# Performance work log

Hardware: AMD Instinct MI355X
Metric: run time of the kernel (lower is better)

## Reference

```python
import jax, jax.numpy as jnp
import numpy as np

RU, RV = 6, 6
DU, DV = 2 * RU + 1, 2 * RV + 1  # 13, 13 displacement offsets
C = 32  # feat_channels (WipModule.c_feat)


def _conv(x, w, stride=1, pad=1):
    return jax.lax.conv_general_dilated(
        x, w, (stride, stride), [(pad, pad), (pad, pad)],
        dimension_numbers=('NCHW', 'OIHW', 'NCHW'))


def _deconv(x, w):
    # expressed as an lhs-dilated conv (kernel stored directly in OIHW conv layout).
    p = 4 - 1 - 1
    return jax.lax.conv_general_dilated(
        x, w, (1, 1), [(p, p), (p, p)], lhs_dilation=(2, 2),
        dimension_numbers=('NCHW', 'OIHW', 'NCHW'))


def _kaiming(key, shape):
    fan_in = shape[1] * shape[2] * shape[3]
    return jax.random.normal(key, shape, jnp.float32) * np.float32(np.sqrt(2.0 / fan_in))


def setup_inputs() -> dict:
    key = jax.random.key(0)
    ks = jax.random.split(key, 8)
    B, H, W = 1, 64, 128
    return {
        'fmap1': jax.random.normal(ks[0], (B, C, H, W), jnp.float32),
        'fmap2': jax.random.normal(ks[1], (B, C, H, W), jnp.float32),
        'w1': _kaiming(ks[2], (96, 2 * C, 3, 3)),
        'w2': _kaiming(ks[3], (128, 96, 3, 3)),
        'w3': _kaiming(ks[4], (128, 128, 3, 3)),
        'w4': _kaiming(ks[5], (64, 128, 3, 3)),
        'wd': _kaiming(ks[6], (32, 64, 4, 4)),
        'w5': _kaiming(ks[7], (1, 32, 3, 3)),
    }


def _build_mvol(fmap1, fmap2):
    # Vectorized form of the torch itertools.product loop: one padded gather
    # over all (du, dv) displacement windows instead of 169 slice-assignments.
    b, c, h, w = fmap1.shape
    padded = jnp.pad(fmap2, ((0, 0), (0, 0), (RV, RV), (RU, RU)))

    def window(i, j):
        # shifted(y, x) = fmap2[y + (j - RV), x + (i - RU)], zero outside bounds
        return jax.lax.dynamic_slice(padded, (0, 0, j, i), (b, c, h, w))

    shifted = jax.vmap(lambda i: jax.vmap(lambda j: window(i, j))(jnp.arange(DV)))(jnp.arange(DU))
    shifted = jnp.moveaxis(shifted, 2, 0)  # (b, du, dv, c, h, w)
    # valid mask: detached channel-sum of the warped fmap2 slice (matches torch)
    valid = (jax.lax.stop_gradient(shifted).sum(axis=3, keepdims=True) != 0)
    valid = valid.astype(fmap1.dtype)
    m1 = fmap1[:, None, None] * valid  # broadcast fmap1 over (du, dv)
    return jnp.concatenate([m1, shifted * valid], axis=3)  # (b, du, dv, 2c, h, w)


def reference(fmap1, fmap2, w1, w2, w3, w4, wd, w5):
    mvol = _build_mvol(fmap1, fmap2)
    b, du, dv, c2, h, w = mvol.shape
    # MatchingNet: fold (du, dv) into batch, conv stack down to 1 cost channel
    x = mvol.reshape(b * du * dv, c2, h, w)
    x = jax.nn.relu(_conv(x, w1))
    x = jax.nn.relu(_conv(x, w2, stride=2))  # (.., 128, h/2, w/2)
    x = jax.nn.relu(_conv(x, w3))
    x = jax.nn.relu(_conv(x, w4))
    x = jax.nn.relu(_deconv(x, wd))          # back to (h, w)
    x = _conv(x, w5)                          # cost, 1 channel
    return x.reshape(b, du, dv, h, w)
```

## Files before the change

### kernel.cpp

```cpp
#include <hip/hip_runtime.h>

#define NITEMS 169

typedef __attribute__((ext_vector_type(8))) __bf16 bf16x8;
typedef __attribute__((ext_vector_type(4))) float f32x4;
typedef __attribute__((ext_vector_type(8))) unsigned short u16x8;
typedef __attribute__((ext_vector_type(4))) unsigned short u16x4;

__device__ __forceinline__ unsigned short f2b(float x) {
  union { float f; unsigned u; } v; v.f = x;
  unsigned r = v.u + 0x7fffu + ((v.u >> 16) & 1u);
  return (unsigned short)(r >> 16);
}
__device__ __forceinline__ float b2f(unsigned short u) {
  union { unsigned u; float f; } v; v.u = ((unsigned)u) << 16;
  return v.f;
}

__global__ __launch_bounds__(256) void k_prepf(const float* __restrict__ f,
                                               unsigned short* __restrict__ fb) {
  const int pix = blockIdx.x * 256 + threadIdx.x;
  const int y = pix >> 7, x = pix & 127;
#pragma unroll
  for (int c = 0; c < 32; ++c)
    fb[(size_t)pix * 32 + c] = f2b(f[(c * 64 + y) * 128 + x]);
}

__global__ void k_prep3x3(const float* __restrict__ w, unsigned short* __restrict__ wp,
                          int Cout, int Cin) {
  int i = blockIdx.x * 256 + threadIdx.x;
  if (i >= Cout * Cin * 9) return;
  int kx = i % 3, t = i / 3;
  int ky = t % 3; t /= 3;
  int cin = t % Cin, cout = t / Cin;
  int tap = ky * 3 + kx;
  wp[(((cin >> 5) * 9 + tap) * Cout + cout) * 32 + (cin & 31)] = f2b(w[i]);
}

__global__ void k_prepwd(const float* __restrict__ w, unsigned short* __restrict__ wp) {
  int i = blockIdx.x * 256 + threadIdx.x;
  if (i >= 32 * 64 * 16) return;
  int kx = i & 3, ky = (i >> 2) & 3, ci = (i >> 4) & 63, cout = i >> 10;
  wp[(((((ci >> 5) * 4 + ky) * 4 + kx) * 32) + cout) * 32 + (ci & 31)] = f2b(w[i]);
}

__global__ __launch_bounds__(256) void k_z1(
    const unsigned short* __restrict__ f1b, const unsigned short* __restrict__ wp,
    float* __restrict__ z1) {
  const int oy0 = blockIdx.x * 2;
  constexpr int WI = 130;
  __shared__ __align__(16) unsigned short X[4][4][WI][8];
  const int wid = threadIdx.x >> 6, lane = threadIdx.x & 63;
  const int lm = lane & 15, lkg = lane >> 4, lk = lkg * 8;

  f32x4 acc[24];
#pragma unroll
  for (int t = 0; t < 24; ++t) acc[t] = f32x4{0.f, 0.f, 0.f, 0.f};

  for (int c = threadIdx.x; c < 4 * 4 * WI; c += 256) {
    const int cig = c & 3, t2 = c >> 2;
    const int col = t2 % WI, r = t2 / WI;
    const int iy = oy0 - 1 + r, ix = col - 1;
    u16x8 v = {0, 0, 0, 0, 0, 0, 0, 0};
    if ((unsigned)iy < 64u && (unsigned)ix < 128u)
      v = *(const u16x8*)&f1b[(size_t)(iy * 128 + ix) * 32 + cig * 8];
    *(u16x8*)&X[r][cig][col][0] = v;
  }
  __syncthreads();
#pragma unroll
  for (int tap = 0; tap < 9; ++tap) {
    const int ky = tap / 3, kx = tap % 3;
    bf16x8 bf[4];
#pragma unroll
    for (int j = 0; j < 4; ++j) {
      const int mt = wid * 4 + j, rw = mt >> 3, mtx = mt & 7;
      bf[j] = *(const bf16x8*)&X[rw + ky][lkg][mtx * 16 + lm + kx][0];
    }
#pragma unroll
    for (int i = 0; i < 6; ++i) {
      bf16x8 af = *(const bf16x8*)&wp[((0 * 9 + tap) * 96 + i * 16 + lm) * 32 + lk];
#pragma unroll
      for (int j = 0; j < 4; ++j)
        acc[i * 4 + j] =
            __builtin_amdgcn_mfma_f32_16x16x32_bf16(af, bf[j], acc[i * 4 + j], 0, 0, 0);
    }
  }
#pragma unroll
  for (int i = 0; i < 6; ++i)
#pragma unroll
    for (int j = 0; j < 4; ++j) {
      const int mt = wid * 4 + j, rw = mt >> 3, mtx = mt & 7;
      const int cout0 = i * 16 + lkg * 4;
      const int m = mtx * 16 + lm;
      *(f32x4*)&z1[(size_t)((oy0 + rw) * 128 + m) * 96 + cout0] = acc[i * 4 + j];
    }
}

__global__ __launch_bounds__(256) void k_z2e(
    const unsigned short* __restrict__ f2b_, const unsigned short* __restrict__ wp,
    float* __restrict__ z2e) {
  const int u = blockIdx.x;
  constexpr int WI = 194;
  __shared__ __align__(16) unsigned short X[3][4][WI][8];
  const int wid = threadIdx.x >> 6, lane = threadIdx.x & 63;
  const int lm = lane & 15, lkg = lane >> 4, lk = lkg * 8;

  f32x4 acc[18];
#pragma unroll
  for (int t = 0; t < 18; ++t) acc[t] = f32x4{0.f, 0.f, 0.f, 0.f};

  for (int c = threadIdx.x; c < 3 * 4 * WI; c += 256) {
    const int cig = c & 3, t2 = c >> 2;
    const int col = t2 % WI, r = t2 / WI;
    const int iy = u + r - 7, ix = col - 7;
    u16x8 v = {0, 0, 0, 0, 0, 0, 0, 0};
    if ((unsigned)iy < 64u && (unsigned)ix < 128u)
      v = *(const u16x8*)&f2b_[(size_t)(iy * 128 + ix) * 32 + cig * 8];
    *(u16x8*)&X[r][cig][col][0] = v;
  }
  __syncthreads();
#pragma unroll
  for (int tap = 0; tap < 9; ++tap) {
    const int ky = tap / 3, kx = tap % 3;
    bf16x8 bf[3];
#pragma unroll
    for (int j = 0; j < 3; ++j) {
      const int mt = wid * 3 + j;
      bf[j] = *(const bf16x8*)&X[ky][lkg][mt * 16 + lm + kx][0];
    }
#pragma unroll
    for (int i = 0; i < 6; ++i) {
      bf16x8 af = *(const bf16x8*)&wp[((1 * 9 + tap) * 96 + i * 16 + lm) * 32 + lk];
#pragma unroll
      for (int j = 0; j < 3; ++j)
        acc[i * 3 + j] =
            __builtin_amdgcn_mfma_f32_16x16x32_bf16(af, bf[j], acc[i * 3 + j], 0, 0, 0);
    }
  }
#pragma unroll
  for (int i = 0; i < 6; ++i)
#pragma unroll
    for (int j = 0; j < 3; ++j) {
      const int v = (wid * 3 + j) * 16 + lm;
      if (v < 140) {
        const int cout0 = i * 16 + lkg * 4;
        *(f32x4*)&z2e[(size_t)(u * 140 + v) * 96 + cout0] = acc[i * 3 + j];
      }
    }
}

__global__ __launch_bounds__(256) void k_crow(
    const unsigned short* __restrict__ f1b, const unsigned short* __restrict__ wp,
    float* __restrict__ crow) {
  const int dyi = blockIdx.x / 7, r = blockIdx.x % 7;
  const int dy = dyi - 6;
  const int ady = dy < 0 ? -dy : dy;
  if (dy == 0 || r >= ady + 1) return;
  const int rowlo = dy > 0 ? 63 - dy : 0;
  const int oy = rowlo + r;
  constexpr int WI = 130;
  __shared__ __align__(16) unsigned short X[3][4][WI][8];
  const int wid = threadIdx.x >> 6, lane = threadIdx.x & 63;
  const int lm = lane & 15, lkg = lane >> 4, lk = lkg * 8;

  f32x4 acc[12];
#pragma unroll
  for (int t = 0; t < 12; ++t) acc[t] = f32x4{0.f, 0.f, 0.f, 0.f};

  for (int c = threadIdx.x; c < 3 * 4 * WI; c += 256) {
    const int cig = c & 3, t2 = c >> 2;
    const int col = t2 % WI, rr = t2 / WI;
    const int iy = oy - 1 + rr, ix = col - 1;
    const bool band = dy > 0 ? (iy >= 64 - dy) : (iy < -dy);
    u16x8 v = {0, 0, 0, 0, 0, 0, 0, 0};
    if (band && (unsigned)iy < 64u && (unsigned)ix < 128u)
      v = *(const u16x8*)&f1b[(size_t)(iy * 128 + ix) * 32 + cig * 8];
    *(u16x8*)&X[rr][cig][col][0] = v;
  }
  __syncthreads();
#pragma unroll
  for (int tap = 0; tap < 9; ++tap) {
    const int ky = tap / 3, kx = tap % 3;
    bf16x8 bf[2];
#pragma unroll
    for (int j = 0; j < 2; ++j)
      bf[j] = *(const bf16x8*)&X[ky][lkg][(wid * 2 + j) * 16 + lm + kx][0];
#pragma unroll
    for (int i = 0; i < 6; ++i) {
      bf16x8 af = *(const bf16x8*)&wp[((0 * 9 + tap) * 96 + i * 16 + lm) * 32 + lk];
#pragma unroll
      for (int j = 0; j < 2; ++j)
        acc[i * 2 + j] =
            __builtin_amdgcn_mfma_f32_16x16x32_bf16(af, bf[j], acc[i * 2 + j], 0, 0, 0);
    }
  }
#pragma unroll
  for (int i = 0; i < 6; ++i)
#pragma unroll
    for (int j = 0; j < 2; ++j) {
      const int cout0 = i * 16 + lkg * 4;
      const int m = (wid * 2 + j) * 16 + lm;
      *(f32x4*)&crow[(size_t)((dyi * 8 + r) * 128 + m) * 96 + cout0] = acc[i * 2 + j];
    }
}

__global__ __launch_bounds__(256) void k_ccol(
    const unsigned short* __restrict__ f1b, const unsigned short* __restrict__ wp,
    float* __restrict__ ccol) {
  const int dxi = blockIdx.x;
  const int dx = dxi - 6;
  const int adx = dx < 0 ? -dx : dx;
  if (dx == 0) return;
  const int ccnt = adx + 1;
  const int collo = dx > 0 ? 127 - dx : 0;
  __shared__ __align__(16) unsigned short X2[9][66][32];
  const int wid = threadIdx.x >> 6, lane = threadIdx.x & 63;
  const int lm = lane & 15, lkg = lane >> 4, lk = lkg * 8;

  for (int t = threadIdx.x; t < 9 * 66 * 4; t += 256) {
    const int cig = t & 3, pos = t >> 2;
    const int rr = pos % 66, cc = pos / 66;
    const int iy = rr - 1, ix = collo - 1 + cc;
    const bool band = dx > 0 ? (ix >= 128 - dx) : (ix < -dx);
    u16x8 v = {0, 0, 0, 0, 0, 0, 0, 0};
    if (band && (unsigned)iy < 64u && (unsigned)ix < 128u)
      v = *(const u16x8*)&f1b[(size_t)(iy * 128 + ix) * 32 + cig * 8];
    *(u16x8*)&X2[cc][rr][cig * 8] = v;
  }
  __syncthreads();
  for (int c = 0; c < ccnt; ++c) {
    f32x4 acc[6];
#pragma unroll
    for (int i = 0; i < 6; ++i) acc[i] = f32x4{0.f, 0.f, 0.f, 0.f};
#pragma unroll
    for (int tap = 0; tap < 9; ++tap) {
      const int ky = tap / 3, kx = tap % 3;
      bf16x8 bf = *(const bf16x8*)&X2[c + kx][wid * 16 + lm + ky][lk];
#pragma unroll
      for (int i = 0; i < 6; ++i) {
        bf16x8 af = *(const bf16x8*)&wp[((0 * 9 + tap) * 96 + i * 16 + lm) * 32 + lk];
        acc[i] = __builtin_amdgcn_mfma_f32_16x16x32_bf16(af, bf, acc[i], 0, 0, 0);
      }
    }
    const int y = wid * 16 + lm;
#pragma unroll
    for (int i = 0; i < 6; ++i) {
      const int cout0 = i * 16 + lkg * 4;
      *(f32x4*)&ccol[(size_t)((dxi * 64 + y) * 8 + c) * 96 + cout0] = acc[i];
    }
  }
}

__device__ __forceinline__ float dot32(const unsigned short* __restrict__ xv,
                                       const unsigned short* __restrict__ wv) {
  float s = 0.f;
#pragma unroll
  for (int cg = 0; cg < 4; ++cg) {
    u16x8 a = *(const u16x8*)&xv[cg * 8];
    u16x8 b = *(const u16x8*)&wv[cg * 8];
#pragma unroll
    for (int e = 0; e < 8; ++e) s += b2f(a[e]) * b2f(b[e]);
  }
  return s;
}

__global__ __launch_bounds__(256) void k_ccorner(
    const unsigned short* __restrict__ f1b, const unsigned short* __restrict__ w1p,
    float* __restrict__ ccor) {
  const int idx = blockIdx.x * 256 + threadIdx.x;
  if (idx >= NITEMS * 64 * 96) return;
  const int co = idx % 96, t = idx / 96;
  const int c = t & 7, r = (t >> 3) & 7, item = t >> 6;
  const int dx = item / 13 - 6, dy = item % 13 - 6;
  if (dx == 0 || dy == 0) return;
  const int ady = dy < 0 ? -dy : dy, adx = dx < 0 ? -dx : dx;
  if (r >= ady + 1 || c >= adx + 1) return;
  const int rowlo = dy > 0 ? 63 - dy : 0;
  const int collo = dx > 0 ? 127 - dx : 0;
  const int oy = rowlo + r, ox = collo + c;
  float acc = 0.f;
#pragma unroll
  for (int ky = 0; ky < 3; ++ky)
#pragma unroll
    for (int kx = 0; kx < 3; ++kx) {
      const int iy = oy - 1 + ky, ix = ox - 1 + kx;
      const bool rb = dy > 0 ? (iy >= 64 - dy) : (iy < -dy);
      const bool cb = dx > 0 ? (ix >= 128 - dx) : (ix < -dx);
      if (rb && cb && (unsigned)iy < 64u && (unsigned)ix < 128u)
        acc += dot32(&f1b[(size_t)(iy * 128 + ix) * 32],
                     &w1p[((ky * 3 + kx) * 96 + co) * 32]);
    }
  ccor[(size_t)(((item * 8 + r) * 8 + c) * 96) + co] = acc;
}

__global__ __launch_bounds__(256) void k_bcorr_rows(
    const unsigned short* __restrict__ f2bp, const unsigned short* __restrict__ w1p,
    float* __restrict__ rtop, float* __restrict__ rbot) {
  const int idx = blockIdx.x * 256 + threadIdx.x;
  if (idx >= 13 * 140 * 96) return;
  const int co = idx % 96, t = idx / 96;
  const int v = t % 140, dyi = t / 140;
  const int dy = dyi - 6;
  const int rt = dy - 1, rb = 64 + dy;
  float at = 0.f, ab = 0.f;
#pragma unroll
  for (int kx = 0; kx < 3; ++kx) {
    const int x2 = v - 7 + kx;
    if ((unsigned)x2 >= 128u) continue;
    if ((unsigned)rt < 64u)
      at += dot32(&f2bp[(size_t)(rt * 128 + x2) * 32],
                  &w1p[((9 + 0 + kx) * 96 + co) * 32]);
    if ((unsigned)rb < 64u)
      ab += dot32(&f2bp[(size_t)(rb * 128 + x2) * 32],
                  &w1p[((9 + 6 + kx) * 96 + co) * 32]);
  }
  rtop[idx] = at;
  rbot[idx] = ab;
}

__global__ __launch_bounds__(256) void k_bcorr_cols(
    const unsigned short* __restrict__ f2bp, const unsigned short* __restrict__ w1p,
    float* __restrict__ clft, float* __restrict__ crgt) {
  const int idx = blockIdx.x * 256 + threadIdx.x;
  if (idx >= 13 * 76 * 96) return;
  const int co = idx % 96, t = idx / 96;
  const int u = t % 76, dxi = t / 76;
  const int dx = dxi - 6;
  const int cl = dx - 1, cr = 128 + dx;
  float al = 0.f, ar = 0.f;
#pragma unroll
  for (int ky = 0; ky < 3; ++ky) {
    const int y2 = u - 7 + ky;
    if ((unsigned)y2 >= 64u) continue;
    if ((unsigned)cl < 128u)
      al += dot32(&f2bp[(size_t)(y2 * 128 + cl) * 32],
                  &w1p[((9 + ky * 3 + 0) * 96 + co) * 32]);
    if ((unsigned)cr < 128u)
      ar += dot32(&f2bp[(size_t)(y2 * 128 + cr) * 32],
                  &w1p[((9 + ky * 3 + 2) * 96 + co) * 32]);
  }
  clft[idx] = al;
  crgt[idx] = ar;
}

__global__ __launch_bounds__(256) void k_bcorr_corn(
    const unsigned short* __restrict__ f2bp, const unsigned short* __restrict__ w1p,
    float* __restrict__ kcorn) {
  const int idx = blockIdx.x * 256 + threadIdx.x;
  if (idx >= NITEMS * 4 * 96) return;
  const int co = idx % 96, t = idx / 96;
  const int corner = t % 4, item = t / 4;
  const int dx = item / 13 - 6, dy = item % 13 - 6;
  const int row = (corner < 2) ? dy - 1 : 64 + dy;
  const int col = (corner & 1) ? 128 + dx : dx - 1;
  const int ky = (corner < 2) ? 0 : 2;
  const int kx = (corner & 1) ? 2 : 0;
  float acc = 0.f;
  if ((unsigned)row < 64u && (unsigned)col < 128u)
    acc = dot32(&f2bp[(size_t)(row * 128 + col) * 32],
                &w1p[((9 + ky * 3 + kx) * 96 + co) * 32]);
  kcorn[idx] = acc;
}

__global__ __launch_bounds__(256) void k_assemble(
    const float* __restrict__ z1, const float* __restrict__ z2e,
    const float* __restrict__ crow, const float* __restrict__ ccol,
    const float* __restrict__ ccor, const float* __restrict__ rtop,
    const float* __restrict__ rbot, const float* __restrict__ clft,
    const float* __restrict__ crgt, const float* __restrict__ kcorn,
    unsigned short* __restrict__ x1, int base) {
  const int y = blockIdx.x, g = blockIdx.y, item = base + g;
  const int dx = item / 13 - 6, dy = item % 13 - 6;
  const int dyi = dy + 6, dxi = dx + 6;
  const int ady = dy < 0 ? -dy : dy, adx = dx < 0 ? -dx : dx;
  const int rowlo = dy > 0 ? 63 - dy : 0;
  const int rowhi = rowlo + (dy ? ady + 1 : 0);
  const int collo = dx > 0 ? 127 - dx : 0;
  const int colhi = collo + (dx ? adx + 1 : 0);
  const bool inrow = (y >= rowlo) && (y < rowhi);
  const int vrow = y + dy + 6;
  unsigned short* op = x1 + (size_t)g * (8192 * 96);

  for (int t = threadIdx.x; t < 128 * 24; t += 256) {
    const int px = t / 24, c0 = (t % 24) * 4;
    const int v = px + dx + 6;
    f32x4 s = *(const f32x4*)&z1[(size_t)(y * 128 + px) * 96 + c0];
    s += *(const f32x4*)&z2e[(size_t)(vrow * 140 + v) * 96 + c0];
    if (inrow)
      s -= *(const f32x4*)&crow[(size_t)((dyi * 8 + y - rowlo) * 128 + px) * 96 + c0];
    if (px >= collo && px < colhi) {
      s -= *(const f32x4*)&ccol[(size_t)((dxi * 64 + y) * 8 + px - collo) * 96 + c0];
      if (inrow)
        s += *(const f32x4*)&ccor[(size_t)(((item * 8 + y - rowlo) * 8) + px - collo) * 96 + c0];
    }
    if (y == 0) s -= *(const f32x4*)&rtop[(size_t)(dyi * 140 + v) * 96 + c0];
    if (y == 63) s -= *(const f32x4*)&rbot[(size_t)(dyi * 140 + v) * 96 + c0];
    if (px == 0) s -= *(const f32x4*)&clft[(size_t)(dxi * 76 + vrow) * 96 + c0];
    if (px == 127) s -= *(const f32x4*)&crgt[(size_t)(dxi * 76 + vrow) * 96 + c0];
    if (y == 0 && px == 0) s += *(const f32x4*)&kcorn[(size_t)item * 384 + 0 * 96 + c0];
    if (y == 0 && px == 127) s += *(const f32x4*)&kcorn[(size_t)item * 384 + 1 * 96 + c0];
    if (y == 63 && px == 0) s += *(const f32x4*)&kcorn[(size_t)item * 384 + 2 * 96 + c0];
    if (y == 63 && px == 127) s += *(const f32x4*)&kcorn[(size_t)item * 384 + 3 * 96 + c0];
    u16x4 o;
#pragma unroll
    for (int e = 0; e < 4; ++e) o[e] = f2b(fmaxf(s[e], 0.f));
    *(u16x4*)&op[(size_t)(y * 128 + px) * 96 + c0] = o;
  }
}

template <int Cin, int Cout, int H, int W, int STRIDE, bool RELU>
__global__ __launch_bounds__(256) void k_convm(
    const unsigned short* __restrict__ xin, const unsigned short* __restrict__ wp,
    unsigned short* __restrict__ xout) {
  constexpr int OH = H / STRIDE, OW = W / STRIDE;
  constexpr int WI = W + 2;
  constexpr int WIH = (WI + 1) / 2;
  constexpr int NC = Cout / 16, NM = OW / 16;
  static_assert(NC % 4 == 0, "cout tiles divisible by 4 waves");
  constexpr int WCT = NC / 4, WMT = NM;
  const int g = blockIdx.y, oy = blockIdx.x;
  const unsigned short* ip = xin + (size_t)g * Cin * H * W;
  unsigned short* op = xout + (size_t)g * Cout * OH * OW;
  __shared__ __align__(16) unsigned short X[3][4][WI][8];
  const int wid = threadIdx.x >> 6, lane = threadIdx.x & 63;
  const int lm = lane & 15, lkg = lane >> 4, lk = lkg * 8;
  const int ct0 = wid * WCT;

  f32x4 acc[WCT * WMT];
#pragma unroll
  for (int t = 0; t < WCT * WMT; ++t) acc[t] = f32x4{0.f, 0.f, 0.f, 0.f};

  for (int cic = 0; cic < Cin / 32; ++cic) {
    __syncthreads();
    for (int c = threadIdx.x; c < 3 * 4 * WI; c += 256) {
      const int cig = c & 3, t2 = c >> 2;
      const int col = t2 % WI, r = t2 / WI;
      const int iy = oy * STRIDE - 1 + r, ix = col - 1;
      const int pcol = (STRIDE == 2) ? ((col >> 1) + (col & 1) * WIH) : col;
      u16x8 v = {0, 0, 0, 0, 0, 0, 0, 0};
      if ((unsigned)iy < (unsigned)H && (unsigned)ix < (unsigned)W)
        v = *(const u16x8*)&ip[(size_t)(iy * W + ix) * Cin + cic * 32 + cig * 8];
      *(u16x8*)&X[r][cig][pcol][0] = v;
    }
    __syncthreads();
#pragma unroll
    for (int tap = 0; tap < 9; ++tap) {
      const int ky = tap / 3, kx = tap % 3;
      bf16x8 bf[WMT];
#pragma unroll
      for (int j = 0; j < WMT; ++j) {
        const int m = j * 16 + lm;
        const int colr = (STRIDE == 2) ? (m + (kx >> 1) + (kx & 1) * WIH) : (m + kx);
        bf[j] = *(const bf16x8*)&X[ky][lkg][colr][0];
      }
#pragma unroll
      for (int i = 0; i < WCT; ++i) {
        const int cout = (ct0 + i) * 16 + lm;
        bf16x8 af = *(const bf16x8*)&wp[((cic * 9 + tap) * Cout + cout) * 32 + lk];
#pragma unroll
        for (int j = 0; j < WMT; ++j)
          acc[i * WMT + j] =
              __builtin_amdgcn_mfma_f32_16x16x32_bf16(af, bf[j], acc[i * WMT + j], 0, 0, 0);
      }
    }
  }
#pragma unroll
  for (int i = 0; i < WCT; ++i)
#pragma unroll
    for (int j = 0; j < WMT; ++j) {
      const int cout0 = (ct0 + i) * 16 + lkg * 4;
      const int m = j * 16 + lm;
      u16x4 pv;
#pragma unroll
      for (int r = 0; r < 4; ++r) {
        float f = acc[i * WMT + j][r];
        if (RELU) f = fmaxf(f, 0.f);
        pv[r] = f2b(f);
      }
      *(u16x4*)&op[(size_t)(oy * OW + m) * Cout + cout0] = pv;
    }
}

__global__ __launch_bounds__(256) void k_deconvm(
    const unsigned short* __restrict__ x4, const unsigned short* __restrict__ wp,
    unsigned short* __restrict__ x5) {
  const int g = blockIdx.y, mrow = blockIdx.x;
  const unsigned short* ip = x4 + (size_t)g * (2048 * 64);
  unsigned short* op = x5 + (size_t)g * (8192 * 32);
  constexpr int WI = 66;
  __shared__ __align__(16) unsigned short X[3][4][WI][8];
  const int wid = threadIdx.x >> 6, lane = threadIdx.x & 63;
  const int a = wid >> 1, b = wid & 1;
  const int lm = lane & 15, lkg = lane >> 4, lk = lkg * 8;
  f32x4 acc[8];
#pragma unroll
  for (int t = 0; t < 8; ++t) acc[t] = f32x4{0.f, 0.f, 0.f, 0.f};

  for (int cic = 0; cic < 2; ++cic) {
    __syncthreads();
    for (int c = threadIdx.x; c < 3 * 4 * WI; c += 256) {
      const int cig = c & 3, t2 = c >> 2;
      const int col = t2 % WI, r = t2 / WI;
      const int iy = mrow - 1 + r, ix = col - 1;
      u16x8 v = {0, 0, 0, 0, 0, 0, 0, 0};
      if ((unsigned)iy < 32u && (unsigned)ix < 64u)
        v = *(const u16x8*)&ip[(size_t)(iy * 64 + ix) * 64 + cic * 32 + cig * 8];
      *(u16x8*)&X[r][cig][col][0] = v;
    }
    __syncthreads();
#pragma unroll
    for (int u = 0; u < 2; ++u)
#pragma unroll
      for (int vv = 0; vv < 2; ++vv) {
        const int r = (a == 0) ? u : u + 1;
        const int ky = (a == 0) ? 2 * u : 2 * u + 1;
        const int s = (b == 0) ? vv : vv + 1;
        const int kx = (b == 0) ? 2 * vv : 2 * vv + 1;
        bf16x8 bf[4];
#pragma unroll
        for (int j = 0; j < 4; ++j)
          bf[j] = *(const bf16x8*)&X[r][lkg][j * 16 + lm + s][0];
#pragma unroll
        for (int i = 0; i < 2; ++i) {
          bf16x8 af =
              *(const bf16x8*)&wp[((((cic * 4 + ky) * 4 + kx) * 32) + i * 16 + lm) * 32 + lk];
#pragma unroll
          for (int j = 0; j < 4; ++j)
            acc[i * 4 + j] =
                __builtin_amdgcn_mfma_f32_16x16x32_bf16(af, bf[j], acc[i * 4 + j], 0, 0, 0);
        }
      }
  }
#pragma unroll
  for (int i = 0; i < 2; ++i)
#pragma unroll
    for (int j = 0; j < 4; ++j) {
      const int cout0 = i * 16 + lkg * 4;
      const int p = j * 16 + lm;
      const int orow = 2 * mrow + a, ocol = 2 * p + b;
      u16x4 pv;
#pragma unroll
      for (int r2 = 0; r2 < 4; ++r2) pv[r2] = f2b(fmaxf(acc[i * 4 + j][r2], 0.f));
      *(u16x4*)&op[(size_t)(orow * 128 + ocol) * 32 + cout0] = pv;
    }
}

__global__ __launch_bounds__(256) void k_conv5m(
    const unsigned short* __restrict__ x5, const float* __restrict__ w5,
    float* __restrict__ out) {
  const int g = blockIdx.y;
  const int pix = blockIdx.x * 256 + threadIdx.x;
  const int y = pix >> 7, x = pix & 127;
  const unsigned short* ip = x5 + (size_t)g * (8192 * 32);
  float s = 0.f;
#pragma unroll
  for (int t = 0; t < 9; ++t) {
    const int yy = y - 1 + t / 3, xx = x - 1 + t % 3;
    if ((unsigned)yy < 64u && (unsigned)xx < 128u) {
#pragma unroll
      for (int cg = 0; cg < 4; ++cg) {
        u16x8 v = *(const u16x8*)&ip[(size_t)(yy * 128 + xx) * 32 + cg * 8];
#pragma unroll
        for (int e = 0; e < 8; ++e) s += b2f(v[e]) * w5[(cg * 8 + e) * 9 + t];
      }
    }
  }
  out[(size_t)g * 8192 + pix] = s;
}

extern "C" void kernel_launch(void* const* d_in, const int* in_sizes, int n_in,
                              void* d_out, int out_size, void* d_ws, size_t ws_size,
                              hipStream_t stream) {
  const float* f1 = (const float*)d_in[0];
  const float* f2 = (const float*)d_in[1];
  const float* w1 = (const float*)d_in[2];
  const float* w2 = (const float*)d_in[3];
  const float* w3 = (const float*)d_in[4];
  const float* w4 = (const float*)d_in[5];
  const float* wd = (const float*)d_in[6];
  const float* w5 = (const float*)d_in[7];
  float* out = (float*)d_out;

  size_t off = 0;
  auto alloc = [&](size_t bytes) {
    void* p = (char*)d_ws + off;
    off += (bytes + 255) / 256 * 256;
    return p;
  };
  unsigned short* f1b = (unsigned short*)alloc(64 * 128 * 32 * 2);
  unsigned short* f2bp = (unsigned short*)alloc(64 * 128 * 32 * 2);
  unsigned short* w1p = (unsigned short*)alloc(2 * 9 * 96 * 32 * 2);
  unsigned short* w2p = (unsigned short*)alloc(3 * 9 * 128 * 32 * 2);
  unsigned short* w3p = (unsigned short*)alloc(4 * 9 * 128 * 32 * 2);
  unsigned short* w4p = (unsigned short*)alloc(4 * 9 * 64 * 32 * 2);
  unsigned short* wdp = (unsigned short*)alloc(2 * 16 * 32 * 32 * 2);
  float* z1 = (float*)alloc((size_t)64 * 128 * 96 * 4);
  float* z2e = (float*)alloc((size_t)76 * 140 * 96 * 4);
  float* crow = (float*)alloc((size_t)13 * 8 * 128 * 96 * 4);
  float* ccol = (float*)alloc((size_t)13 * 64 * 8 * 96 * 4);
  float* ccor = (float*)alloc((size_t)NITEMS * 8 * 8 * 96 * 4);
  float* rtop = (float*)alloc((size_t)13 * 140 * 96 * 4);
  float* rbot = (float*)alloc((size_t)13 * 140 * 96 * 4);
  float* clft = (float*)alloc((size_t)13 * 76 * 96 * 4);
  float* crgt = (float*)alloc((size_t)13 * 76 * 96 * 4);
  float* kcorn = (float*)alloc((size_t)NITEMS * 4 * 96 * 4);
  const size_t wend = off;

  const size_t perA = (size_t)96 * 8192 * 2;
  const size_t perB = (size_t)128 * 2048 * 2;
  int G = (int)((ws_size - wend) / (perA + perB));
  if (G > NITEMS) G = NITEMS;
  if (G < 1) G = 1;
  unsigned short* A = (unsigned short*)((char*)d_ws + wend);
  unsigned short* B = (unsigned short*)((char*)d_ws + wend + (size_t)G * perA);

  k_prepf<<<32, 256, 0, stream>>>(f1, f1b);
  k_prepf<<<32, 256, 0, stream>>>(f2, f2bp);
  k_prep3x3<<<(96 * 64 * 9 + 255) / 256, 256, 0, stream>>>(w1, w1p, 96, 64);
  k_prep3x3<<<(128 * 96 * 9 + 255) / 256, 256, 0, stream>>>(w2, w2p, 128, 96);
  k_prep3x3<<<(128 * 128 * 9 + 255) / 256, 256, 0, stream>>>(w3, w3p, 128, 128);
  k_prep3x3<<<(64 * 128 * 9 + 255) / 256, 256, 0, stream>>>(w4, w4p, 64, 128);
  k_prepwd<<<(32 * 64 * 16 + 255) / 256, 256, 0, stream>>>(wd, wdp);

  k_z1<<<32, 256, 0, stream>>>(f1b, w1p, z1);
  k_z2e<<<76, 256, 0, stream>>>(f2bp, w1p, z2e);
  k_crow<<<91, 256, 0, stream>>>(f1b, w1p, crow);
  k_ccol<<<13, 256, 0, stream>>>(f1b, w1p, ccol);
  k_ccorner<<<(NITEMS * 64 * 96 + 255) / 256, 256, 0, stream>>>(f1b, w1p, ccor);
  k_bcorr_rows<<<(13 * 140 * 96 + 255) / 256, 256, 0, stream>>>(f2bp, w1p, rtop, rbot);
  k_bcorr_cols<<<(13 * 76 * 96 + 255) / 256, 256, 0, stream>>>(f2bp, w1p, clft, crgt);
  k_bcorr_corn<<<(NITEMS * 4 * 96 + 255) / 256, 256, 0, stream>>>(f2bp, w1p, kcorn);

  for (int base = 0; base < NITEMS; base += G) {
    const int cnt = (NITEMS - base < G) ? (NITEMS - base) : G;
    k_assemble<<<dim3(64, cnt), 256, 0, stream>>>(z1, z2e, crow, ccol, ccor, rtop, rbot,
                                                  clft, crgt, kcorn, A, base);
    k_convm<96, 128, 64, 128, 2, true><<<dim3(32, cnt), 256, 0, stream>>>(A, w2p, B);
    k_convm<128, 128, 32, 64, 1, true><<<dim3(32, cnt), 256, 0, stream>>>(B, w3p, A);
    k_convm<128, 64, 32, 64, 1, true><<<dim3(32, cnt), 256, 0, stream>>>(A, w4p, B);
    k_deconvm<<<dim3(32, cnt), 256, 0, stream>>>(B, wdp, A);
    k_conv5m<<<dim3(32, cnt), 256, 0, stream>>>(A, w5, out + (size_t)base * 8192);
  }
}
```

Before: 742.5 us.

## Fuse first-layer activation assembly into the stride-2 conv2 kernel

Removes the separate assembly kernel that wrote the bf16 first-layer activations to global memory. The stride-2 conv now rebuilds each needed input row on the fly from the precomputed fp32 partial sums and boundary corrections as it loads its shared-memory tile. This eliminates a large intermediate write and read per displacement item and lets more items fit in the workspace. In exchange, overlapping input rows are recomputed across neighbouring output-row blocks, and the tile loads now gather fp32 data with many branches.

```diff
diff --git a/kernel.cpp b/kernel.cpp
--- a/kernel.cpp
+++ b/kernel.cpp
@@ -362,50 +362,128 @@
   kcorn[idx] = acc;
 }
 
-__global__ __launch_bounds__(256) void k_assemble(
+struct ItemGeo {
+  int item, dx, dy, dyi, dxi, rowlo, rowhi, collo, colhi;
+};
+
+__device__ __forceinline__ u16x8 x1_fuse8(
     const float* __restrict__ z1, const float* __restrict__ z2e,
     const float* __restrict__ crow, const float* __restrict__ ccol,
     const float* __restrict__ ccor, const float* __restrict__ rtop,
     const float* __restrict__ rbot, const float* __restrict__ clft,
     const float* __restrict__ crgt, const float* __restrict__ kcorn,
-    unsigned short* __restrict__ x1, int base) {
-  const int y = blockIdx.x, g = blockIdx.y, item = base + g;
-  const int dx = item / 13 - 6, dy = item % 13 - 6;
-  const int dyi = dy + 6, dxi = dx + 6;
-  const int ady = dy < 0 ? -dy : dy, adx = dx < 0 ? -dx : dx;
-  const int rowlo = dy > 0 ? 63 - dy : 0;
-  const int rowhi = rowlo + (dy ? ady + 1 : 0);
-  const int collo = dx > 0 ? 127 - dx : 0;
-  const int colhi = collo + (dx ? adx + 1 : 0);
-  const bool inrow = (y >= rowlo) && (y < rowhi);
-  const int vrow = y + dy + 6;
-  unsigned short* op = x1 + (size_t)g * (8192 * 96);
-
-  for (int t = threadIdx.x; t < 128 * 24; t += 256) {
-    const int px = t / 24, c0 = (t % 24) * 4;
-    const int v = px + dx + 6;
-    f32x4 s = *(const f32x4*)&z1[(size_t)(y * 128 + px) * 96 + c0];
-    s += *(const f32x4*)&z2e[(size_t)(vrow * 140 + v) * 96 + c0];
+    const ItemGeo& gm, int y, int px, int c0) {
+  const bool inrow = (y >= gm.rowlo) && (y < gm.rowhi);
+  const bool incol = (px >= gm.collo) && (px < gm.colhi);
+  const int vrow = y + gm.dy + 6;
+  const int v = px + gm.dx + 6;
+  u16x8 o;
+#pragma unroll
+  for (int h = 0; h < 2; ++h) {
+    const int cc = c0 + h * 4;
+    f32x4 s = *(const f32x4*)&z1[(size_t)(y * 128 + px) * 96 + cc];
+    s += *(const f32x4*)&z2e[(size_t)(vrow * 140 + v) * 96 + cc];
     if (inrow)
-      s -= *(const f32x4*)&crow[(size_t)((dyi * 8 + y - rowlo) * 128 + px) * 96 + c0];
-    if (px >= collo && px < colhi) {
-      s -= *(const f32x4*)&ccol[(size_t)((dxi * 64 + y) * 8 + px - collo) * 96 + c0];
+      s -= *(const f32x4*)&crow[(size_t)((gm.dyi * 8 + y - gm.rowlo) * 128 + px) * 96 + cc];
+    if (incol) {
+      s -= *(const f32x4*)&ccol[(size_t)((gm.dxi * 64 + y) * 8 + px - gm.collo) * 96 + cc];
       if (inrow)
-        s += *(const f32x4*)&ccor[(size_t)(((item * 8 + y - rowlo) * 8) + px - collo) * 96 + c0];
-    }
-    if (y == 0) s -= *(const f32x4*)&rtop[(size_t)(dyi * 140 + v) * 96 + c0];
-    if (y == 63) s -= *(const f32x4*)&rbot[(size_t)(dyi * 140 + v) * 96 + c0];
-    if (px == 0) s -= *(const f32x4*)&clft[(size_t)(dxi * 76 + vrow) * 96 + c0];
-    if (px == 127) s -= *(const f32x4*)&crgt[(size_t)(dxi * 76 + vrow) * 96 + c0];
-    if (y == 0 && px == 0) s += *(const f32x4*)&kcorn[(size_t)item * 384 + 0 * 96 + c0];
-    if (y == 0 && px == 127) s += *(const f32x4*)&kcorn[(size_t)item * 384 + 1 * 96 + c0];
-    if (y == 63 && px == 0) s += *(const f32x4*)&kcorn[(size_t)item * 384 + 2 * 96 + c0];
-    if (y == 63 && px == 127) s += *(const f32x4*)&kcorn[(size_t)item * 384 + 3 * 96 + c0];
-    u16x4 o;
-#pragma unroll
-    for (int e = 0; e < 4; ++e) o[e] = f2b(fmaxf(s[e], 0.f));
-    *(u16x4*)&op[(size_t)(y * 128 + px) * 96 + c0] = o;
-  }
+        s += *(const f32x4*)&ccor[(size_t)(((gm.item * 8 + y - gm.rowlo) * 8) + px - gm.collo) * 96 + cc];
+    }
+    if (y == 0) s -= *(const f32x4*)&rtop[(size_t)(gm.dyi * 140 + v) * 96 + cc];
+    if (y == 63) s -= *(const f32x4*)&rbot[(size_t)(gm.dyi * 140 + v) * 96 + cc];
+    if (px == 0) s -= *(const f32x4*)&clft[(size_t)(gm.dxi * 76 + vrow) * 96 + cc];
+    if (px == 127) s -= *(const f32x4*)&crgt[(size_t)(gm.dxi * 76 + vrow) * 96 + cc];
+    if (y == 0 && px == 0) s += *(const f32x4*)&kcorn[(size_t)gm.item * 384 + 0 * 96 + cc];
+    if (y == 0 && px == 127) s += *(const f32x4*)&kcorn[(size_t)gm.item * 384 + 1 * 96 + cc];
+    if (y == 63 && px == 0) s += *(const f32x4*)&kcorn[(size_t)gm.item * 384 + 2 * 96 + cc];
+    if (y == 63 && px == 127) s += *(const f32x4*)&kcorn[(size_t)gm.item * 384 + 3 * 96 + cc];
+#pragma unroll
+    for (int e = 0; e < 4; ++e) o[h * 4 + e] = f2b(fmaxf(s[e], 0.f));
+  }
+  return o;
+}
+
+__global__ __launch_bounds__(256) void k_conv2f(
+    const float* __restrict__ z1, const float* __restrict__ z2e,
+    const float* __restrict__ crow, const float* __restrict__ ccol,
+    const float* __restrict__ ccor, const float* __restrict__ rtop,
+    const float* __restrict__ rbot, const float* __restrict__ clft,
+    const float* __restrict__ crgt, const float* __restrict__ kcorn,
+    const unsigned short* __restrict__ wp, unsigned short* __restrict__ x2,
+    int base) {
+  constexpr int WI = 130, WIH = 65;
+  const int g = blockIdx.y, oy = blockIdx.x;
+  const int item = base + g;
+  ItemGeo gm;
+  gm.item = item;
+  gm.dx = item / 13 - 6;
+  gm.dy = item % 13 - 6;
+  gm.dyi = gm.dy + 6;
+  gm.dxi = gm.dx + 6;
+  {
+    const int ady = gm.dy < 0 ? -gm.dy : gm.dy, adx = gm.dx < 0 ? -gm.dx : gm.dx;
+    gm.rowlo = gm.dy > 0 ? 63 - gm.dy : 0;
+    gm.rowhi = gm.rowlo + (gm.dy ? ady + 1 : 0);
+    gm.collo = gm.dx > 0 ? 127 - gm.dx : 0;
+    gm.colhi = gm.collo + (gm.dx ? adx + 1 : 0);
+  }
+  unsigned short* op = x2 + (size_t)g * (128 * 2048);
+  __shared__ __align__(16) unsigned short X[3][4][WI][8];
+  const int wid = threadIdx.x >> 6, lane = threadIdx.x & 63;
+  const int lm = lane & 15, lkg = lane >> 4, lk = lkg * 8;
+  const int ct0 = wid * 2;
+
+  f32x4 acc[8];
+#pragma unroll
+  for (int t = 0; t < 8; ++t) acc[t] = f32x4{0.f, 0.f, 0.f, 0.f};
+
+  for (int cic = 0; cic < 3; ++cic) {
+    __syncthreads();
+    for (int c = threadIdx.x; c < 3 * 4 * WI; c += 256) {
+      const int cig = c & 3, t2 = c >> 2;
+      const int col = t2 % WI, r = t2 / WI;
+      const int iy = oy * 2 - 1 + r, ix = col - 1;
+      const int pcol = (col >> 1) + (col & 1) * WIH;
+      u16x8 v = {0, 0, 0, 0, 0, 0, 0, 0};
+      if ((unsigned)iy < 64u && (unsigned)ix < 128u)
+        v = x1_fuse8(z1, z2e, crow, ccol, ccor, rtop, rbot, clft, crgt, kcorn,
+                     gm, iy, ix, cic * 32 + cig * 8);
+      *(u16x8*)&X[r][cig][pcol][0] = v;
+    }
+    __syncthreads();
+#pragma unroll
+    for (int tap = 0; tap < 9; ++tap) {
+      const int ky = tap / 3, kx = tap % 3;
+      bf16x8 bf[4];
+#pragma unroll
+      for (int j = 0; j < 4; ++j) {
+        const int m = j * 16 + lm;
+        const int colr = m + (kx >> 1) + (kx & 1) * WIH;
+        bf[j] = *(const bf16x8*)&X[ky][lkg][colr][0];
+      }
+#pragma unroll
+      for (int i = 0; i < 2; ++i) {
+        const int cout = (ct0 + i) * 16 + lm;
+        bf16x8 af = *(const bf16x8*)&wp[((cic * 9 + tap) * 128 + cout) * 32 + lk];
+#pragma unroll
+        for (int j = 0; j < 4; ++j)
+          acc[i * 4 + j] =
+              __builtin_amdgcn_mfma_f32_16x16x32_bf16(af, bf[j], acc[i * 4 + j], 0, 0, 0);
+      }
+    }
+  }
+#pragma unroll
+  for (int i = 0; i < 2; ++i)
+#pragma unroll
+    for (int j = 0; j < 4; ++j) {
+      const int cout0 = (ct0 + i) * 16 + lkg * 4;
+      const int m = j * 16 + lm;
+      u16x4 pv;
+#pragma unroll
+      for (int r = 0; r < 4; ++r) pv[r] = f2b(fmaxf(acc[i * 4 + j][r], 0.f));
+      *(u16x4*)&op[(size_t)(oy * 64 + m) * 128 + cout0] = pv;
+    }
 }
 
 template <int Cin, int Cout, int H, int W, int STRIDE, bool RELU>
@@ -606,13 +684,12 @@
   float* kcorn = (float*)alloc((size_t)NITEMS * 4 * 96 * 4);
   const size_t wend = off;
 
-  const size_t perA = (size_t)96 * 8192 * 2;
-  const size_t perB = (size_t)128 * 2048 * 2;
-  int G = (int)((ws_size - wend) / (perA + perB));
+  const size_t perSlot = (size_t)128 * 2048 * 2;
+  int G = (int)((ws_size - wend) / (2 * perSlot));
   if (G > NITEMS) G = NITEMS;
   if (G < 1) G = 1;
-  unsigned short* A = (unsigned short*)((char*)d_ws + wend);
-  unsigned short* B = (unsigned short*)((char*)d_ws + wend + (size_t)G * perA);
+  unsigned short* P = (unsigned short*)((char*)d_ws + wend);
+  unsigned short* Q = (unsigned short*)((char*)d_ws + wend + (size_t)G * perSlot);
 
   k_prepf<<<32, 256, 0, stream>>>(f1, f1b);
   k_prepf<<<32, 256, 0, stream>>>(f2, f2bp);
@@ -633,12 +710,11 @@
 
   for (int base = 0; base < NITEMS; base += G) {
     const int cnt = (NITEMS - base < G) ? (NITEMS - base) : G;
-    k_assemble<<<dim3(64, cnt), 256, 0, stream>>>(z1, z2e, crow, ccol, ccor, rtop, rbot,
-                                                  clft, crgt, kcorn, A, base);
-    k_convm<96, 128, 64, 128, 2, true><<<dim3(32, cnt), 256, 0, stream>>>(A, w2p, B);
-    k_convm<128, 128, 32, 64, 1, true><<<dim3(32, cnt), 256, 0, stream>>>(B, w3p, A);
-    k_convm<128, 64, 32, 64, 1, true><<<dim3(32, cnt), 256, 0, stream>>>(A, w4p, B);
-    k_deconvm<<<dim3(32, cnt), 256, 0, stream>>>(B, wdp, A);
-    k_conv5m<<<dim3(32, cnt), 256, 0, stream>>>(A, w5, out + (size_t)base * 8192);
-  }
-}
+    k_conv2f<<<dim3(32, cnt), 256, 0, stream>>>(z1, z2e, crow, ccol, ccor, rtop, rbot,
+                                                clft, crgt, kcorn, w2p, P, base);
+    k_convm<128, 128, 32, 64, 1, true><<<dim3(32, cnt), 256, 0, stream>>>(P, w3p, Q);
+    k_convm<128, 64, 32, 64, 1, true><<<dim3(32, cnt), 256, 0, stream>>>(Q, w4p, P);
+    k_deconvm<<<dim3(32, cnt), 256, 0, stream>>>(P, wdp, Q);
+    k_conv5m<<<dim3(32, cnt), 256, 0, stream>>>(Q, w5, out + (size_t)base * 8192);
+  }
+}
```

New measurement: 702.9 us. 1.06x faster.
